# Optimization experiments

Hardware: AMD Instinct MI355X
Metric: run time of the kernel (lower is better)

The kernel has to match this reference:

```python
import math
import jax
import jax.numpy as jnp
import numpy as np

B = 2; Hrv = 16; Wrv = 1024; Crv = 64; Cb = 128; Cout = 128
D = 128; K = 5; NH = 8; NP = 4; DH = D // NH
Hbev = 220; Wbev = 220
RMAX = 55.0; XMIN = -55.0; XMAX = 55.0; YMIN = -55.0; YMAX = 55.0
EDGE_GAIN = 4.0; KLW = 1e-4

ELEV = np.array([-30.67, -29.33, -28.0, -26.66, -25.33, -24.0, -22.67, -21.33, -20.0, -18.67, -17.33, -16.0, -14.67, -13.33, -12.0, -10.67, -9.33, -8.0, -6.66, -5.33, -4.0, -2.67, -1.33, 0.0, 1.33, 2.67, 4.0, 5.33, 6.67, 8.0, 9.33, 10.67], dtype=np.float32)


def _buffers():
    groups = ELEV[::-1].reshape(Hrv, 32 // Hrv)
    steps = np.deg2rad(groups.max(1) - groups.min(1)).astype(np.float32)
    # torch Tensor.repeat == tile (faithful to original, even though rows end up interleaved)
    elev_steps = np.tile(steps, Wrv).reshape(Hrv, Wrv)
    means = np.deg2rad(groups.mean(1)).astype(np.float32)
    elevation = np.repeat(means, Wrv).reshape(Hrv, Wrv)  # numpy repeat == elementwise
    az_line = np.linspace(-np.pi, np.pi, Wrv + 1, dtype=np.float64)[:-1]
    az_step = float(az_line[1] - az_line[0])
    az_line = (az_line + az_step / 2).astype(np.float32)
    azimuth = np.broadcast_to(az_line[None, :], (Hrv, Wrv)).astype(np.float32).copy()
    offsets = np.linspace(-0.6, 0.6, K).astype(np.float32)
    u_vec = np.stack([np.cos(elevation) * np.cos(azimuth), np.cos(elevation) * np.sin(azimuth), np.sin(elevation)], 0).astype(np.float32)
    return (jnp.asarray(elev_steps), jnp.asarray(elevation), jnp.asarray(azimuth), az_step, jnp.asarray(offsets), jnp.asarray(u_vec))


def conv1x1(x, w, b):
    return jnp.einsum('bchw,oc->bohw', x, w) + b[None, :, None, None]


def groupnorm(x, g, gamma, beta, eps=1e-5):
    b_, c, h, w = x.shape
    xr = x.reshape(b_, g, c // g, h, w)
    m = xr.mean(axis=(2, 3, 4), keepdims=True)
    v = xr.var(axis=(2, 3, 4), keepdims=True)
    xn = ((xr - m) * jax.lax.rsqrt(v + eps)).reshape(b_, c, h, w)
    return xn * gamma[None, :, None, None] + beta[None, :, None, None]


def bilinear_sample(v_t, loc, H, W):
    # v_t: [B,NH,H*W,DH]; loc: [B,Nq,NH,NP,2] in [0,1]; grid_sample align_corners=False, zeros pad
    x = loc[..., 0] * W - 0.5
    y = loc[..., 1] * H - 0.5
    x0 = jnp.floor(x); y0 = jnp.floor(y)
    wx = x - x0; wy = y - y0
    x0i = x0.astype(jnp.int32); y0i = y0.astype(jnp.int32)
    b_, n_, nh_, p_ = x.shape

    def gather(xi, yi):
        valid = (xi >= 0) & (xi < W) & (yi >= 0) & (yi < H)
        idx = jnp.clip(yi, 0, H - 1) * W + jnp.clip(xi, 0, W - 1)
        idx_t = idx.transpose(0, 2, 1, 3).reshape(b_, nh_, n_ * p_)
        g = jnp.take_along_axis(v_t, idx_t[..., None], axis=2).reshape(b_, nh_, n_, p_, -1)
        return g * valid.transpose(0, 2, 1, 3)[..., None]

    wxt = wx.transpose(0, 2, 1, 3)[..., None]
    wyt = wy.transpose(0, 2, 1, 3)[..., None]
    g = gather(x0i, y0i) * (1 - wxt) * (1 - wyt)
    g = g + gather(x0i + 1, y0i) * wxt * (1 - wyt)
    g = g + gather(x0i, y0i + 1) * (1 - wxt) * wyt
    g = g + gather(x0i + 1, y0i + 1) * wxt * wyt
    return g  # [B,NH,Nq,NP,DH]


def setup_inputs():
    key = jax.random.key(0)
    ks = jax.random.split(key, 20)
    def rn(k, shape, s=0.02):
        return jax.random.normal(k, shape, jnp.float32) * s
    inp = {}
    inp['x_rv'] = jax.random.normal(ks[0], (B, Hrv, Wrv, Crv), jnp.float32)
    inp['bev'] = jax.random.normal(ks[1], (B, Cb, Hbev, Wbev), jnp.float32)
    inp['lidar2ego_mat'] = jnp.eye(4, dtype=jnp.float32)[None] + 0.01 * jax.random.normal(ks[2], (1, 4, 4), jnp.float32)
    inp['w_q'] = rn(ks[3], (D, Crv)); inp['b_q'] = jnp.zeros((D,), jnp.float32)
    inp['w_v'] = rn(ks[4], (D, Cb)); inp['b_v'] = jnp.zeros((D,), jnp.float32)
    inp['w_o'] = rn(ks[5], (Cout, D)); inp['b_o'] = jnp.zeros((Cout,), jnp.float32)
    inp['qs_w1'] = rn(ks[6], (D, D + 6)); inp['qs_b1'] = jnp.zeros((D,), jnp.float32)
    inp['qs_w2'] = rn(ks[7], (D, D)); inp['qs_b2'] = jnp.zeros((D,), jnp.float32)
    inp['rh_w1'] = rn(ks[8], (128, Crv + 3)); inp['rh_b1'] = jnp.zeros((128,), jnp.float32)
    inp['rh_g1'] = jnp.ones((128,), jnp.float32); inp['rh_bt1'] = jnp.zeros((128,), jnp.float32)
    inp['rh_w2'] = rn(ks[9], (64, 128, 3, 3))
    inp['rh_g2'] = jnp.ones((64,), jnp.float32); inp['rh_bt2'] = jnp.zeros((64,), jnp.float32)
    inp['rh_w3'] = rn(ks[10], (4, 64)); inp['rh_b3'] = jnp.zeros((4,), jnp.float32)
    inp['off_w'] = rn(ks[11], (NH * K * NP * 2, D)); inp['off_b'] = rn(ks[12], (NH * K * NP * 2,), 0.5)
    inp['aw_w'] = rn(ks[13], (NH * K * NP, D)); inp['aw_b'] = jnp.zeros((NH * K * NP,), jnp.float32)
    inp['val_w'] = rn(ks[14], (D, D)); inp['val_b'] = jnp.zeros((D,), jnp.float32)
    inp['out_w'] = rn(ks[15], (D, D)); inp['out_b'] = jnp.zeros((D,), jnp.float32)
    return inp


def reference(x_rv, bev, lidar2ego_mat, w_q, b_q, w_v, b_v, w_o, b_o, qs_w1, qs_b1, qs_w2, qs_b2, rh_w1, rh_b1, rh_g1, rh_bt1, rh_w2, rh_g2, rh_bt2, rh_w3, rh_b3, off_w, off_b, aw_w, aw_b, val_w, val_b, out_w, out_b):
    elev_steps, elevation, azimuth, az_step, offsets, u_vec = _buffers()
    x = jnp.transpose(x_rv, (0, 3, 1, 2))  # [B,Crv,Hrv,Wrv]
    Q0 = conv1x1(x, w_q, b_q)
    Vmap = conv1x1(bev, w_v, b_v)
    range_in = jnp.concatenate([x, jnp.broadcast_to(u_vec[None], (B, 3, Hrv, Wrv))], axis=1)
    h = jax.nn.gelu(groupnorm(conv1x1(range_in, rh_w1, rh_b1), 8, rh_g1, rh_bt1), approximate=False)
    hp = jnp.pad(h, ((0, 0), (0, 0), (1, 1), (1, 1)), mode='wrap')  # circular padding
    h = jax.lax.conv_general_dilated(hp, rh_w2, (1, 1), 'VALID', dimension_numbers=('NCHW', 'OIHW', 'NCHW'))
    h = jax.nn.gelu(groupnorm(h, 8, rh_g2, rh_bt2), approximate=False)
    head = conv1x1(h, rh_w3, rh_b3)  # [B,4,Hrv,Wrv]
    mu = jax.nn.sigmoid(head[:, 0:1]) * RMAX
    sd = jax.nn.softplus(head[:, 1:2]) + 1e-3
    se = jax.nn.sigmoid(head[:, 2:3]) * elev_steps + 1e-3
    sa = jax.nn.sigmoid(head[:, 3:4]) * az_step + 1e-3
    depth = mu[:, 0][..., None] + sd[:, 0][..., None] * offsets  # [B,Hrv,Wrv,K]
    elevs = elevation[None, :, :, None] + se[:, 0][..., None] * offsets
    azs = azimuth[None, :, :, None] + sa[:, 0][..., None] * offsets
    ce = jnp.cos(elevs)
    x_l = depth * ce * jnp.cos(azs)
    y_l = depth * ce * jnp.sin(azs)
    z_l = depth * jnp.sin(elevs)
    NK = Hrv * Wrv * K
    p = jnp.stack([x_l.reshape(B, NK), y_l.reshape(B, NK), z_l.reshape(B, NK), jnp.ones((B, NK), x_l.dtype)], axis=-1)
    p_ego = jnp.matmul(p, lidar2ego_mat)  # [B,NK,4]
    rx = jax.nn.sigmoid(EDGE_GAIN * ((p_ego[..., 0] - XMIN) / (XMAX - XMIN) - 0.5))
    ry = jax.nn.sigmoid(EDGE_GAIN * ((p_ego[..., 1] - YMIN) / (YMAX - YMIN) - 0.5))
    ref = jnp.stack([rx, ry], axis=-1).reshape(B, Hrv * Wrv, K, 2)
    sig_feat = jnp.concatenate([sd, se, sa, 1.0 / (sd + 1e-6), 1.0 / (se + 1e-6), 1.0 / (sa + 1e-6)], axis=1)
    Q = conv1x1(jax.nn.gelu(conv1x1(jnp.concatenate([Q0, sig_feat], axis=1), qs_w1, qs_b1), approximate=False), qs_w2, qs_b2)
    query = jnp.transpose(Q, (0, 2, 3, 1)).reshape(B, Hrv * Wrv, D)
    value = jnp.transpose(Vmap.reshape(B, D, Hbev * Wbev), (0, 2, 1))  # [B,HW,D]
    # MSDA -- all K levels share the same BEV value map (value was repeat(1,K,1))
    v = (value @ val_w.T + val_b).reshape(B, Hbev * Wbev, NH, DH)
    v_t = jnp.transpose(v, (0, 2, 1, 3))  # [B,NH,HW,DH]
    Nq = Hrv * Wrv
    smp_off = (query @ off_w.T + off_b).reshape(B, Nq, NH, K, NP, 2)
    attn = jax.nn.softmax((query @ aw_w.T + aw_b).reshape(B, Nq, NH, K * NP), axis=-1).reshape(B, Nq, NH, K, NP)
    norm = jnp.array([Wbev, Hbev], jnp.float32)
    loc = ref[:, :, None, :, None, :] + smp_off / norm  # [B,Nq,NH,K,NP,2]
    out = jnp.zeros((B, Nq, NH, DH), jnp.float32)
    for l in range(K):
        smp = bilinear_sample(v_t, loc[:, :, :, l], Hbev, Wbev)
        out = out + jnp.einsum('bhnpd,bnhp->bnhd', smp, attn[:, :, :, l])
    y_msda = out.reshape(B, Nq, D) @ out_w.T + out_b + query  # mmcv identity residual
    y = jnp.transpose(y_msda.reshape(B, Hrv, Wrv, D), (0, 3, 1, 2))
    y = conv1x1(y, w_o, b_o)
    mu_norm = mu / RMAX
    sr = jnp.maximum(sd, 1e-6)
    saz = sa / az_step
    sel = se / elev_steps
    L_kl = 0.5 * (mu_norm ** 2 + sr ** 2 - jnp.log(sr ** 2) - 1.0) \
         + 0.5 * (saz ** 2 - jnp.log(saz ** 2) - 1.0) \
         + 0.5 * (sel ** 2 - jnp.log(sel ** 2) - 1.0)
    kl = KLW * L_kl.mean()
    y = y.reshape(B, Hrv, Wrv, -1)  # faithful to torch .view on NCHW (no permute)
    return (y, kl)
```

## Files before the change

kernel.cpp:

```cpp
#include <hip/hip_runtime.h>
#include <math.h>

#define HRV 16
#define WRV 1024
#define NPIX 16384
#define NBEV 48400
#define BSZ 2

typedef __attribute__((ext_vector_type(8))) short short8;
typedef __attribute__((ext_vector_type(4))) float f32x4;

struct RVConsts {
  float steps[16];
  float means[16];
  float az_step_f;
  float pad_;
  double step_d;
  double az0;
  double az_half;
};

__device__ __forceinline__ float geluf(float x) {
  return 0.5f * x * (1.0f + erff(x * 0.70710678118654752440f));
}
__device__ __forceinline__ float sigmoidf_(float x) {
  return 1.0f / (1.0f + expf(-x));
}
__device__ __forceinline__ float softplusf_(float x) {
  return fmaxf(x, 0.0f) + log1pf(expf(-fabsf(x)));
}
__device__ __forceinline__ float azimf(int w, double step_d, double az0, double az_half) {
  double az = (double)w * step_d + az0;
  az += az_half;
  return (float)az;
}
__device__ __forceinline__ unsigned short f2bf(float f) {
  unsigned int u = __builtin_bit_cast(unsigned int, f);
  u = u + 0x7FFFu + ((u >> 16) & 1u);
  return (unsigned short)(u >> 16);
}
__device__ __forceinline__ float bf2f(unsigned short h) {
  unsigned int u = ((unsigned int)h) << 16;
  return __builtin_bit_cast(float, u);
}

__global__ __launch_bounds__(256) void k_rh1_q0(
    const float* __restrict__ x_rv,
    const unsigned short* __restrict__ rhW1p, const float* __restrict__ rh_b1,
    const unsigned short* __restrict__ wqp, const float* __restrict__ b_q,
    float* __restrict__ t1, unsigned short* __restrict__ q0,
    float* __restrict__ sums1, RVConsts C) {
  __shared__ unsigned short xin[64][104];
  __shared__ float wred[4][8][2];
  int b = blockIdx.y;
  int n0 = blockIdx.x * 64;
  int tid = threadIdx.x;
  const float* src = x_rv + ((size_t)b * NPIX + n0) * 64;
  for (int i = tid; i < 1024; i += 256) {
    int p = i >> 4, c = (i & 15) * 4;
    float4 v4 = *(const float4*)(src + p * 64 + c);
    xin[p][c] = f2bf(v4.x);
    xin[p][c + 1] = f2bf(v4.y);
    xin[p][c + 2] = f2bf(v4.z);
    xin[p][c + 3] = f2bf(v4.w);
  }
  if (tid < 64) {
    int n = n0 + tid;
    int h = n >> 10, w = n & 1023;
    float E = C.means[h];
    float A = azimf(w, C.step_d, C.az0, C.az_half);
    float ce = cosf(E);
    xin[tid][64] = f2bf(ce * cosf(A));
    xin[tid][65] = f2bf(ce * sinf(A));
    xin[tid][66] = f2bf(sinf(E));
    for (int c = 67; c < 104; c++) xin[tid][c] = 0;
  }
  __syncthreads();
  int wave = tid >> 6, l = tid & 63;
  int lr = l & 15, lk = l >> 4;
  f32x4 acc[8], accq[8];
#pragma unroll
  for (int nt = 0; nt < 8; nt++) {
    float b1 = rh_b1[nt * 16 + lr], b2 = b_q[nt * 16 + lr];
    acc[nt] = (f32x4){b1, b1, b1, b1};
    accq[nt] = (f32x4){b2, b2, b2, b2};
  }
#pragma unroll
  for (int ks = 0; ks < 3; ks++) {
    short8 a = *(const short8*)&xin[wave * 16 + lr][ks * 32 + lk * 8];
#pragma unroll
    for (int nt = 0; nt < 8; nt++) {
      short8 b1v = *(const short8*)(rhW1p + (size_t)(nt * 16 + lr) * 96 + ks * 32 + lk * 8);
      acc[nt] = __builtin_amdgcn_mfma_f32_16x16x32_bf16(a, b1v, acc[nt], 0, 0, 0);
      short8 b2v = *(const short8*)(wqp + (size_t)(nt * 16 + lr) * 96 + ks * 32 + lk * 8);
      accq[nt] = __builtin_amdgcn_mfma_f32_16x16x32_bf16(a, b2v, accq[nt], 0, 0, 0);
    }
  }
#pragma unroll
  for (int nt = 0; nt < 8; nt++) {
    int n = nt * 16 + lr;
#pragma unroll
    for (int r = 0; r < 4; r++) {
      int p = n0 + wave * 16 + lk * 4 + r;
      size_t o = ((size_t)b * NPIX + p) * 128 + n;
      t1[o] = acc[nt][r];
      q0[o] = f2bf(accq[nt][r]);
    }
  }
  float s1[8], ss1[8];
#pragma unroll
  for (int nt = 0; nt < 8; nt++) {
    float a0 = acc[nt][0], a1 = acc[nt][1], a2 = acc[nt][2], a3 = acc[nt][3];
    s1[nt] = a0 + a1 + a2 + a3;
    ss1[nt] = a0 * a0 + a1 * a1 + a2 * a2 + a3 * a3;
  }
#pragma unroll
  for (int nt = 0; nt < 8; nt++) {
    s1[nt] += __shfl_xor(s1[nt], 1);  ss1[nt] += __shfl_xor(ss1[nt], 1);
    s1[nt] += __shfl_xor(s1[nt], 2);  ss1[nt] += __shfl_xor(ss1[nt], 2);
    s1[nt] += __shfl_xor(s1[nt], 4);  ss1[nt] += __shfl_xor(ss1[nt], 4);
    s1[nt] += __shfl_xor(s1[nt], 8);  ss1[nt] += __shfl_xor(ss1[nt], 8);
    s1[nt] += __shfl_xor(s1[nt], 16); ss1[nt] += __shfl_xor(ss1[nt], 16);
    s1[nt] += __shfl_xor(s1[nt], 32); ss1[nt] += __shfl_xor(ss1[nt], 32);
  }
  if (l == 0) {
#pragma unroll
    for (int nt = 0; nt < 8; nt++) { wred[wave][nt][0] = s1[nt]; wred[wave][nt][1] = ss1[nt]; }
  }
  __syncthreads();
  if (tid < 8) {
    float S = wred[0][tid][0] + wred[1][tid][0] + wred[2][tid][0] + wred[3][tid][0];
    float SS = wred[0][tid][1] + wred[1][tid][1] + wred[2][tid][1] + wred[3][tid][1];
    sums1[(((size_t)b * 8 + tid) * 256 + blockIdx.x) * 2 + 0] = S;
    sums1[(((size_t)b * 8 + tid) * 256 + blockIdx.x) * 2 + 1] = SS;
  }
}

__device__ __forceinline__ int cswz2(int row, int colw, int c) {
  int byte = ((row * 10 + colw) << 8) + (c << 1);
  return byte ^ ((row & 7) << 4);
}
__global__ __launch_bounds__(256) void k_conv3g(
    const float* __restrict__ t1, const float* __restrict__ sums1,
    const float* __restrict__ g1, const float* __restrict__ bt1,
    const unsigned short* __restrict__ w2p,
    float* __restrict__ t2, float* __restrict__ sums2) {
  __shared__ unsigned short tile[16 * 10 * 128];
  __shared__ float st[8][2];
  __shared__ float wred[4][2][4][2];
  int b = blockIdx.y;
  int w0 = blockIdx.x * 8;
  int tid = threadIdx.x;
  if (tid < 8) {
    int g = tid;
    float S = 0.f, SS = 0.f;
    for (int ch = 0; ch < 256; ch++) {
      S += sums1[(((size_t)b * 8 + g) * 256 + ch) * 2];
      SS += sums1[(((size_t)b * 8 + g) * 256 + ch) * 2 + 1];
    }
    float m = S * (1.0f / 262144.0f);
    float var = SS * (1.0f / 262144.0f) - m * m;
    st[g][0] = m;
    st[g][1] = rsqrtf(var + 1e-5f);
  }
  __syncthreads();
  for (int i = tid; i < 5120; i += 256) {
    int row = i / 320;
    int rem = i - row * 320;
    int colw = rem >> 5;
    int c4 = (rem & 31) * 4;
    int wc = (w0 + colw - 1 + WRV) & (WRV - 1);
    float4 x4 = *(const float4*)(t1 + ((size_t)b * NPIX + row * WRV + wc) * 128 + c4);
    int g = c4 >> 4;
    float m = st[g][0], is = st[g][1];
    float4 g4 = *(const float4*)(g1 + c4);
    float4 b4 = *(const float4*)(bt1 + c4);
    float y0 = geluf((x4.x - m) * is * g4.x + b4.x);
    float y1 = geluf((x4.y - m) * is * g4.y + b4.y);
    float y2 = geluf((x4.z - m) * is * g4.z + b4.z);
    float y3 = geluf((x4.w - m) * is * g4.w + b4.w);
    uint2 o;
    o.x = (unsigned int)f2bf(y0) | ((unsigned int)f2bf(y1) << 16);
    o.y = (unsigned int)f2bf(y2) | ((unsigned int)f2bf(y3) << 16);
    *(uint2*)((char*)tile + cswz2(row, colw, c4)) = o;
  }
  __syncthreads();
  int wave = tid >> 6, l = tid & 63;
  int lr = l & 15, lk = l >> 4;
  f32x4 acc[2][4];
#pragma unroll
  for (int cc2 = 0; cc2 < 2; cc2++)
#pragma unroll
    for (int nt = 0; nt < 4; nt++) acc[cc2][nt] = (f32x4){0.f, 0.f, 0.f, 0.f};
#pragma unroll
  for (int kpos = 0; kpos < 9; kpos++) {
    int ky = kpos / 3, kx = kpos - ky * 3;
    int arow = (lr + ky - 1 + 16) & 15;
#pragma unroll
    for (int cc2 = 0; cc2 < 2; cc2++) {
      int acol = wave * 2 + cc2 + kx;
#pragma unroll
      for (int ks = 0; ks < 4; ks++) {
        short8 a = *(const short8*)((const char*)tile + cswz2(arow, acol, ks * 32 + lk * 8));
#pragma unroll
        for (int nt = 0; nt < 4; nt++) {
          short8 bv = *(const short8*)(w2p + (size_t)(kpos * 64 + nt * 16 + lr) * 128 +
                                       ks * 32 + lk * 8);
          acc[cc2][nt] = __builtin_amdgcn_mfma_f32_16x16x32_bf16(a, bv, acc[cc2][nt], 0, 0, 0);
        }
      }
    }
  }
#pragma unroll
  for (int cc2 = 0; cc2 < 2; cc2++) {
    int cc = wave * 2 + cc2;
#pragma unroll
    for (int nt = 0; nt < 4; nt++) {
      int o = nt * 16 + lr;
#pragma unroll
      for (int r = 0; r < 4; r++) {
        int p = (lk * 4 + r) * WRV + w0 + cc;
        t2[((size_t)b * NPIX + p) * 64 + o] = acc[cc2][nt][r];
      }
    }
  }
  float ps[4], pss[4];
#pragma unroll
  for (int nt = 0; nt < 4; nt++) { ps[nt] = 0.f; pss[nt] = 0.f; }
#pragma unroll
  for (int cc2 = 0; cc2 < 2; cc2++)
#pragma unroll
    for (int nt = 0; nt < 4; nt++)
#pragma unroll
      for (int r = 0; r < 4; r++) {
        float v = acc[cc2][nt][r];
        ps[nt] += v;
        pss[nt] += v * v;
      }
#pragma unroll
  for (int nt = 0; nt < 4; nt++) {
    ps[nt] += __shfl_xor(ps[nt], 1);  pss[nt] += __shfl_xor(pss[nt], 1);
    ps[nt] += __shfl_xor(ps[nt], 2);  pss[nt] += __shfl_xor(pss[nt], 2);
    ps[nt] += __shfl_xor(ps[nt], 4);  pss[nt] += __shfl_xor(pss[nt], 4);
    ps[nt] += __shfl_xor(ps[nt], 16); pss[nt] += __shfl_xor(pss[nt], 16);
    ps[nt] += __shfl_xor(ps[nt], 32); pss[nt] += __shfl_xor(pss[nt], 32);
  }
  if ((l & 0x37) == 0) {
    int b3 = (l >> 3) & 1;
#pragma unroll
    for (int nt = 0; nt < 4; nt++) {
      wred[wave][b3][nt][0] = ps[nt];
      wred[wave][b3][nt][1] = pss[nt];
    }
  }
  __syncthreads();
  if (tid < 8) {
    int nt = tid >> 1, b3 = tid & 1;
    float S = 0.f, SS = 0.f;
    for (int wv = 0; wv < 4; wv++) { S += wred[wv][b3][nt][0]; SS += wred[wv][b3][nt][1]; }
    int g = nt * 2 + b3;
    sums2[(((size_t)b * 8 + g) * 128 + blockIdx.x) * 2 + 0] = S;
    sums2[(((size_t)b * 8 + g) * 128 + blockIdx.x) * 2 + 1] = SS;
  }
}

__global__ __launch_bounds__(256) void k_headquery(
    const float* __restrict__ t2, const float* __restrict__ sums2,
    const float* __restrict__ g2, const float* __restrict__ bt2,
    const float* __restrict__ rh_w3, const float* __restrict__ rh_b3,
    const float* __restrict__ l2e, const unsigned short* __restrict__ q0,
    const unsigned short* __restrict__ qsW1p, const float* __restrict__ qs_b1,
    const float* __restrict__ qs_w1f,
    const unsigned short* __restrict__ qsW2p, const float* __restrict__ qs_b2,
    float* __restrict__ params, float* __restrict__ klpart,
    unsigned short* __restrict__ query, RVConsts C) {
  __shared__ float st2[8][2];
  __shared__ unsigned short qin[64][136];
  __shared__ unsigned short hq[64][136];
  __shared__ float sigf[64][6];
  __shared__ float klred[64];
  int b = blockIdx.y;
  int n0 = blockIdx.x * 64;
  int tid = threadIdx.x;
  if (tid < 8) {
    int g = tid;
    float S = 0.f, SS = 0.f;
    for (int ch = 0; ch < 128; ch++) {
      S += sums2[(((size_t)b * 8 + g) * 128 + ch) * 2];
      SS += sums2[(((size_t)b * 8 + g) * 128 + ch) * 2 + 1];
    }
    float m = S * (1.0f / 131072.0f);
    float var = SS * (1.0f / 131072.0f) - m * m;
    st2[g][0] = m;
    st2[g][1] = rsqrtf(var + 1e-5f);
  }
  const unsigned short* src = q0 + ((size_t)b * NPIX + n0) * 128;
  for (int i = tid; i < 1024; i += 256) {
    int p = i >> 4, c0 = (i & 15) * 8;
    *(uint4*)&qin[p][c0] = *(const uint4*)(src + p * 128 + c0);
  }
  __syncthreads();
  {
    int px = tid >> 2, q = tid & 3;
    int n = n0 + px;
    int h = n >> 10, w = n & 1023;
    const float* t = t2 + ((size_t)b * NPIX + n) * 64 + q * 16;
    float hd0 = 0.f, hd1 = 0.f, hd2 = 0.f, hd3 = 0.f;
#pragma unroll
    for (int j = 0; j < 16; j++) {
      int c = q * 16 + j;
      int g = c >> 3;
      float xv = geluf((t[j] - st2[g][0]) * st2[g][1] * g2[c] + bt2[c]);
      hd0 += rh_w3[c] * xv;
      hd1 += rh_w3[64 + c] * xv;
      hd2 += rh_w3[128 + c] * xv;
      hd3 += rh_w3[192 + c] * xv;
    }
    hd0 += __shfl_xor(hd0, 1); hd1 += __shfl_xor(hd1, 1);
    hd2 += __shfl_xor(hd2, 1); hd3 += __shfl_xor(hd3, 1);
    hd0 += __shfl_xor(hd0, 2); hd1 += __shfl_xor(hd1, 2);
    hd2 += __shfl_xor(hd2, 2); hd3 += __shfl_xor(hd3, 2);
    if (q == 0) {
      hd0 += rh_b3[0]; hd1 += rh_b3[1]; hd2 += rh_b3[2]; hd3 += rh_b3[3];
      float mu = sigmoidf_(hd0) * 55.0f;
      float sd = softplusf_(hd1) + 1e-3f;
      float stepw = C.steps[w & 15];
      float se = sigmoidf_(hd2) * stepw + 1e-3f;
      float sa = sigmoidf_(hd3) * C.az_step_f + 1e-3f;
      float E0 = C.means[h];
      float A0 = azimf(w, C.step_d, C.az0, C.az_half);
      float* P = params + ((size_t)b * NPIX + n) * 16;
      P[0] = sd; P[1] = se; P[2] = sa;
      sigf[px][0] = sd; sigf[px][1] = se; sigf[px][2] = sa;
      sigf[px][3] = 1.0f / (sd + 1e-6f);
      sigf[px][4] = 1.0f / (se + 1e-6f);
      sigf[px][5] = 1.0f / (sa + 1e-6f);
      float M00 = l2e[0], M01 = l2e[1], M10 = l2e[4], M11 = l2e[5];
      float M20 = l2e[8], M21 = l2e[9], M30 = l2e[12], M31 = l2e[13];
#pragma unroll
      for (int k = 0; k < 5; k++) {
        float off = -0.6f + 0.3f * (float)k;
        float d = mu + sd * off;
        float E = E0 + se * off;
        float A = A0 + sa * off;
        float ce = cosf(E);
        float xl = d * ce * cosf(A), yl = d * ce * sinf(A), zl = d * sinf(E);
        float px_ = xl * M00 + yl * M10 + zl * M20 + M30;
        float py_ = xl * M01 + yl * M11 + zl * M21 + M31;
        P[3 + 2 * k] = sigmoidf_(4.0f * ((px_ + 55.0f) * (1.0f / 110.0f) - 0.5f));
        P[4 + 2 * k] = sigmoidf_(4.0f * ((py_ + 55.0f) * (1.0f / 110.0f) - 0.5f));
      }
      float mu_n = mu * (1.0f / 55.0f);
      float sr = fmaxf(sd, 1e-6f);
      float saz = sa / C.az_step_f;
      float sel = se / stepw;
      klred[px] = 0.5f * (mu_n * mu_n + sr * sr - logf(sr * sr) - 1.0f) +
                  0.5f * (saz * saz - logf(saz * saz) - 1.0f) +
                  0.5f * (sel * sel - logf(sel * sel) - 1.0f);
    }
  }
  __syncthreads();
  if (tid == 0) {
    float sL = 0.f;
    for (int i = 0; i < 64; i++) sL += klred[i];
    klpart[b * 256 + blockIdx.x] = sL;
  }
  int wave = tid >> 6, l = tid & 63;
  int lr = l & 15, lk = l >> 4;
  f32x4 acc[8];
#pragma unroll
  for (int nt = 0; nt < 8; nt++) {
    int n = nt * 16 + lr;
    float wt[6];
#pragma unroll
    for (int c = 0; c < 6; c++) wt[c] = qs_w1f[(size_t)n * 134 + 128 + c];
    float bias = qs_b1[n];
#pragma unroll
    for (int r = 0; r < 4; r++) {
      int pl = wave * 16 + lk * 4 + r;
      float a = bias;
#pragma unroll
      for (int c = 0; c < 6; c++) a += wt[c] * sigf[pl][c];
      acc[nt][r] = a;
    }
  }
#pragma unroll
  for (int ks = 0; ks < 4; ks++) {
    short8 a = *(const short8*)&qin[wave * 16 + lr][ks * 32 + lk * 8];
#pragma unroll
    for (int nt = 0; nt < 8; nt++) {
      short8 bv = *(const short8*)(qsW1p + (size_t)(nt * 16 + lr) * 128 + ks * 32 + lk * 8);
      acc[nt] = __builtin_amdgcn_mfma_f32_16x16x32_bf16(a, bv, acc[nt], 0, 0, 0);
    }
  }
#pragma unroll
  for (int nt = 0; nt < 8; nt++)
#pragma unroll
    for (int r = 0; r < 4; r++)
      hq[wave * 16 + lk * 4 + r][nt * 16 + lr] = f2bf(geluf(acc[nt][r]));
  __syncthreads();
#pragma unroll
  for (int nt = 0; nt < 8; nt++) {
    float bias = qs_b2[nt * 16 + lr];
    acc[nt] = (f32x4){bias, bias, bias, bias};
  }
#pragma unroll
  for (int ks = 0; ks < 4; ks++) {
    short8 a = *(const short8*)&hq[wave * 16 + lr][ks * 32 + lk * 8];
#pragma unroll
    for (int nt = 0; nt < 8; nt++) {
      short8 bv = *(const short8*)(qsW2p + (size_t)(nt * 16 + lr) * 128 + ks * 32 + lk * 8);
      acc[nt] = __builtin_amdgcn_mfma_f32_16x16x32_bf16(a, bv, acc[nt], 0, 0, 0);
    }
  }
#pragma unroll
  for (int nt = 0; nt < 8; nt++) {
    int n = nt * 16 + lr;
#pragma unroll
    for (int r = 0; r < 4; r++) {
      int p = n0 + wave * 16 + lk * 4 + r;
      query[((size_t)b * NPIX + p) * 128 + n] = f2bf(acc[nt][r]);
    }
  }
}

__global__ __launch_bounds__(256) void k_pack(
    const float* __restrict__ val_w, const float* __restrict__ w_v,
    const float* __restrict__ b_v, const float* __restrict__ val_b,
    const float* __restrict__ off_w, const float* __restrict__ off_b,
    const float* __restrict__ aw_w, const float* __restrict__ aw_b,
    const float* __restrict__ out_w, const float* __restrict__ qs_w1,
    const float* __restrict__ qs_w2, const float* __restrict__ rh_w1,
    const float* __restrict__ w_q, const float* __restrict__ w_o,
    const float* __restrict__ rh_w2,
    unsigned short* __restrict__ wvv_bf, float* __restrict__ bvv,
    unsigned short* __restrict__ projW, float* __restrict__ projB,
    unsigned short* __restrict__ outW, unsigned short* __restrict__ qsW1p,
    unsigned short* __restrict__ qsW2p, unsigned short* __restrict__ rhW1p,
    unsigned short* __restrict__ wqp, unsigned short* __restrict__ woP,
    unsigned short* __restrict__ w2p) {
  int idx = blockIdx.x * 256 + threadIdx.x;
  if (idx < 16384) {
    int o = idx >> 7, c = idx & 127;
    float acc = 0.0f;
    for (int m = 0; m < 128; m++) acc += val_w[o * 128 + m] * w_v[m * 128 + c];
    wvv_bf[idx] = f2bf(acc);
  } else if (idx < 16512) {
    int o = idx - 16384;
    float acc = val_b[o];
    for (int m = 0; m < 128; m++) acc += val_w[o * 128 + m] * b_v[m];
    bvv[o] = acc;
  } else if (idx < 82048) {
    int j = idx - 16512;
    int r = j >> 7, c = j & 127;
    float w = (r < 320) ? off_w[r * 128 + c] : ((r < 480) ? aw_w[(r - 320) * 128 + c] : 0.0f);
    projW[j] = f2bf(w);
  } else if (idx < 82560) {
    int r = idx - 82048;
    projB[r] = (r < 320) ? off_b[r] : ((r < 480) ? aw_b[r - 320] : 0.0f);
  } else if (idx < 98944) {
    int j = idx - 82560;
    outW[j] = f2bf(out_w[j]);
  } else if (idx < 115328) {
    int j = idx - 98944;
    int r = j >> 7, c = j & 127;
    qsW1p[j] = f2bf(qs_w1[r * 134 + c]);
  } else if (idx < 131712) {
    int j = idx - 115328;
    qsW2p[j] = f2bf(qs_w2[j]);
  } else if (idx < 144000) {
    int j = idx - 131712;
    int r = j / 96, c = j - r * 96;
    rhW1p[j] = (c < 67) ? f2bf(rh_w1[r * 67 + c]) : 0;
  } else if (idx < 156288) {
    int j = idx - 144000;
    int r = j / 96, c = j - r * 96;
    wqp[j] = (c < 64) ? f2bf(w_q[r * 64 + c]) : 0;
  } else if (idx < 172672) {
    int j = idx - 156288;
    woP[j] = f2bf(w_o[j]);
  } else if (idx < 246400) {
    int j = idx - 172672;
    int kpos = j >> 13;
    int rem = j & 8191;
    int o = rem >> 7, c = rem & 127;
    int ky = kpos / 3, kx = kpos - ky * 3;
    w2p[j] = f2bf(rh_w2[((size_t)(o * 128 + c) * 3 + ky) * 3 + kx]);
  }
}

__global__ __launch_bounds__(256) void k_value(
    const float* __restrict__ bev, const unsigned short* __restrict__ wvv_bf,
    const float* __restrict__ bvv, unsigned short* __restrict__ v) {
  __shared__ float lds[128 * 66];
  int b = blockIdx.y;
  int p0 = blockIdx.x * 64;
  int tid = threadIdx.x;
  int npx = NBEV - p0; if (npx > 64) npx = 64;
  for (int i = tid; i < 128 * 64; i += 256) {
    int c = i >> 6, p = i & 63;
    lds[c * 66 + p] = (p < npx) ? bev[((size_t)b * 128 + c) * NBEV + p0 + p] : 0.0f;
  }
  __syncthreads();
  int wave = tid >> 6, l = tid & 63;
  int lr = l & 15, lk = l >> 4;
  int ploc = wave * 16 + lr;
  f32x4 acc[8];
#pragma unroll
  for (int nt = 0; nt < 8; nt++) {
    float bias = bvv[nt * 16 + lr];
    acc[nt] = (f32x4){bias, bias, bias, bias};
  }
#pragma unroll
  for (int ks = 0; ks < 4; ks++) {
    int k0 = ks * 32 + lk * 8;
    short8 a;
#pragma unroll
    for (int j = 0; j < 8; j++) a[j] = (short)f2bf(lds[(k0 + j) * 66 + ploc]);
#pragma unroll
    for (int nt = 0; nt < 8; nt++) {
      short8 bf = *(const short8*)(wvv_bf + (size_t)(nt * 16 + lr) * 128 + k0);
      acc[nt] = __builtin_amdgcn_mfma_f32_16x16x32_bf16(a, bf, acc[nt], 0, 0, 0);
    }
  }
#pragma unroll
  for (int nt = 0; nt < 8; nt++) {
    int n = nt * 16 + lr;
#pragma unroll
    for (int r = 0; r < 4; r++) {
      int p = p0 + wave * 16 + lk * 4 + r;
      if (p < NBEV) v[((size_t)b * NBEV + p) * 128 + n] = f2bf(acc[nt][r]);
    }
  }
}

__global__ __launch_bounds__(256) void k_proj(
    const unsigned short* __restrict__ query, const unsigned short* __restrict__ projW,
    const float* __restrict__ projB, unsigned short* __restrict__ proj) {
  __shared__ unsigned short qlds[64][136];
  int b = blockIdx.y;
  int p0b = blockIdx.x * 64;
  int tid = threadIdx.x;
  const unsigned short* src = query + ((size_t)b * NPIX + p0b) * 128;
  for (int i = tid; i < 1024; i += 256) {
    int p = i >> 4, c0 = (i & 15) * 8;
    *(uint4*)&qlds[p][c0] = *(const uint4*)(src + p * 128 + c0);
  }
  __syncthreads();
  int wave = tid >> 6, l = tid & 63;
  int lr = l & 15, lk = l >> 4;
  int p0 = p0b + wave * 16;
  for (int nc = 0; nc < 4; nc++) {
    int n0 = nc * 128;
    f32x4 acc[8];
#pragma unroll
    for (int nt = 0; nt < 8; nt++) {
      float bias = projB[n0 + nt * 16 + lr];
      acc[nt] = (f32x4){bias, bias, bias, bias};
    }
#pragma unroll
    for (int ks = 0; ks < 4; ks++) {
      short8 a = *(const short8*)&qlds[wave * 16 + lr][ks * 32 + lk * 8];
#pragma unroll
      for (int nt = 0; nt < 8; nt++) {
        short8 bf = *(const short8*)(projW + (size_t)(n0 + nt * 16 + lr) * 128 +
                                     ks * 32 + lk * 8);
        acc[nt] = __builtin_amdgcn_mfma_f32_16x16x32_bf16(a, bf, acc[nt], 0, 0, 0);
      }
    }
#pragma unroll
    for (int nt = 0; nt < 8; nt++) {
      int n = n0 + nt * 16 + lr;
#pragma unroll
      for (int r = 0; r < 4; r++) {
        int p = p0 + lk * 4 + r;
        proj[((size_t)b * NPIX + p) * 512 + n] = f2bf(acc[nt][r]);
      }
    }
  }
}

__global__ __launch_bounds__(256) void k_samp(
    const unsigned short* __restrict__ proj, const float* __restrict__ params,
    const unsigned short* __restrict__ v, unsigned short* __restrict__ S) {
  int b = blockIdx.y;
  int bid = blockIdx.x;
  int pb = (bid & 7) * 512 + (bid >> 3);
  int tid = threadIdx.x;
  int g = tid & 7;
  int hh = (tid >> 3) & 7;
  int pl = tid >> 6;
  int ts = g >> 1, th = g & 1;
  int n = pb * 4 + pl;
  const unsigned short* base = proj + ((size_t)b * NPIX + n) * 512;
  float lg[5];
#pragma unroll
  for (int t = 0; t < 5; t++) lg[t] = bf2f(base[320 + hh * 20 + ts * 5 + t]);
  float mx = fmaxf(fmaxf(fmaxf(lg[0], lg[1]), fmaxf(lg[2], lg[3])), lg[4]);
  mx = fmaxf(mx, __shfl_xor(mx, 2));
  mx = fmaxf(mx, __shfl_xor(mx, 4));
  float e[5];
  float s = 0.0f;
#pragma unroll
  for (int t = 0; t < 5; t++) { e[t] = expf(lg[t] - mx); s += e[t]; }
  s += __shfl_xor(s, 2);
  s += __shfl_xor(s, 4);
  float rs = 1.0f / s;
  const float* P = params + ((size_t)b * NPIX + n) * 16;
  const unsigned short* vb = v + (size_t)b * NBEV * 128 + hh * 16 + th * 8;
  float acc[8];
#pragma unroll
  for (int c = 0; c < 8; c++) acc[c] = 0.0f;
#pragma unroll
  for (int t = 0; t < 5; t++) {
    int kp = ts * 5 + t;
    int k = kp >> 2;
    unsigned int u = *(const unsigned int*)(base + hh * 40 + kp * 2);
    float X = P[3 + 2 * k] * 220.0f - 0.5f + bf2f((unsigned short)(u & 0xffffu));
    float Y = P[4 + 2 * k] * 220.0f - 0.5f + bf2f((unsigned short)(u >> 16));
    float xf = floorf(X), yf = floorf(Y);
    float wx = X - xf, wy = Y - yf;
    int x0 = (int)xf, y0 = (int)yf;
    float wx0 = ((unsigned)x0 < 220u) ? (1.0f - wx) : 0.0f;
    float wx1 = ((unsigned)(x0 + 1) < 220u) ? wx : 0.0f;
    float wy0 = ((unsigned)y0 < 220u) ? (1.0f - wy) : 0.0f;
    float wy1 = ((unsigned)(y0 + 1) < 220u) ? wy : 0.0f;
    int cx0 = min(max(x0, 0), 219), cx1 = min(max(x0 + 1, 0), 219);
    int cy0 = min(max(y0, 0), 219) * 220, cy1 = min(max(y0 + 1, 0), 219) * 220;
    float a = e[t] * rs;
    float u0 = a * wy0, u1 = a * wy1;
    float w4[4] = {u0 * wx0, u0 * wx1, u1 * wx0, u1 * wx1};
    int i4[4] = {cy0 + cx0, cy0 + cx1, cy1 + cx0, cy1 + cx1};
#pragma unroll
    for (int c2 = 0; c2 < 4; c2++) {
      float w = w4[c2];
      const uint2* sp = (const uint2*)(vb + (size_t)i4[c2] * 128);
      uint2 r0 = sp[0], r1 = sp[1];
      acc[0] += w * bf2f((unsigned short)(r0.x & 0xffffu));
      acc[1] += w * bf2f((unsigned short)(r0.x >> 16));
      acc[2] += w * bf2f((unsigned short)(r0.y & 0xffffu));
      acc[3] += w * bf2f((unsigned short)(r0.y >> 16));
      acc[4] += w * bf2f((unsigned short)(r1.x & 0xffffu));
      acc[5] += w * bf2f((unsigned short)(r1.x >> 16));
      acc[6] += w * bf2f((unsigned short)(r1.y & 0xffffu));
      acc[7] += w * bf2f((unsigned short)(r1.y >> 16));
    }
  }
#pragma unroll
  for (int c = 0; c < 8; c++) {
    acc[c] += __shfl_xor(acc[c], 2);
    acc[c] += __shfl_xor(acc[c], 4);
  }
  if (ts == 0) {
    uint4 o1;
    o1.x = (unsigned int)f2bf(acc[0]) | ((unsigned int)f2bf(acc[1]) << 16);
    o1.y = (unsigned int)f2bf(acc[2]) | ((unsigned int)f2bf(acc[3]) << 16);
    o1.z = (unsigned int)f2bf(acc[4]) | ((unsigned int)f2bf(acc[5]) << 16);
    o1.w = (unsigned int)f2bf(acc[6]) | ((unsigned int)f2bf(acc[7]) << 16);
    *(uint4*)(S + ((size_t)b * NPIX + n) * 128 + hh * 16 + th * 8) = o1;
  }
}

__global__ __launch_bounds__(256) void k_outfinal(
    const unsigned short* __restrict__ S, const unsigned short* __restrict__ outW,
    const float* __restrict__ out_b, const unsigned short* __restrict__ query,
    const unsigned short* __restrict__ woP, const float* __restrict__ b_o,
    const float* __restrict__ klpart, float* __restrict__ out) {
  __shared__ unsigned short ylds[64][136];
  __shared__ float yt[128][67];
  int b = blockIdx.y;
  int p0b = blockIdx.x * 64;
  int tid = threadIdx.x;
  int wave = tid >> 6, l = tid & 63;
  int lr = l & 15, lk = l >> 4;
  {
    f32x4 acc[8];
#pragma unroll
    for (int nt = 0; nt < 8; nt++) {
      float bias = out_b[nt * 16 + lr];
      acc[nt] = (f32x4){bias, bias, bias, bias};
    }
    const unsigned short* ap = S + ((size_t)b * NPIX + p0b + wave * 16 + lr) * 128 + lk * 8;
#pragma unroll
    for (int ks = 0; ks < 4; ks++) {
      short8 a = *(const short8*)(ap + ks * 32);
#pragma unroll
      for (int nt = 0; nt < 8; nt++) {
        short8 bf = *(const short8*)(outW + (size_t)(nt * 16 + lr) * 128 + ks * 32 + lk * 8);
        acc[nt] = __builtin_amdgcn_mfma_f32_16x16x32_bf16(a, bf, acc[nt], 0, 0, 0);
      }
    }
#pragma unroll
    for (int nt = 0; nt < 8; nt++) {
      int n = nt * 16 + lr;
#pragma unroll
      for (int r = 0; r < 4; r++) {
        int p_local = wave * 16 + lk * 4 + r;
        size_t o = ((size_t)b * NPIX + p0b + p_local) * 128 + n;
        ylds[p_local][n] = f2bf(acc[nt][r] + bf2f(query[o]));
      }
    }
  }
  __syncthreads();
  {
    f32x4 acc[8];
#pragma unroll
    for (int nt = 0; nt < 8; nt++) {
      float bias = b_o[nt * 16 + lr];
      acc[nt] = (f32x4){bias, bias, bias, bias};
    }
#pragma unroll
    for (int ks = 0; ks < 4; ks++) {
      short8 a = *(const short8*)&ylds[wave * 16 + lr][ks * 32 + lk * 8];
#pragma unroll
      for (int nt = 0; nt < 8; nt++) {
        short8 bf = *(const short8*)(woP + (size_t)(nt * 16 + lr) * 128 + ks * 32 + lk * 8);
        acc[nt] = __builtin_amdgcn_mfma_f32_16x16x32_bf16(a, bf, acc[nt], 0, 0, 0);
      }
    }
#pragma unroll
    for (int nt = 0; nt < 8; nt++)
#pragma unroll
      for (int r = 0; r < 4; r++)
        yt[nt * 16 + lr][wave * 16 + lk * 4 + r] = acc[nt][r];
  }
  __syncthreads();
  int n = tid >> 1, half = tid & 1;
  float* dst = out + ((size_t)(b * 128 + n)) * NPIX + p0b + half * 32;
#pragma unroll
  for (int j = 0; j < 8; j++) {
    float4 v4 = {yt[n][half * 32 + j * 4], yt[n][half * 32 + j * 4 + 1],
                 yt[n][half * 32 + j * 4 + 2], yt[n][half * 32 + j * 4 + 3]};
    *(float4*)(dst + j * 4) = v4;
  }
  if (blockIdx.x == 0 && b == 0 && tid == 0) {
    float sL = 0.0f;
    for (int i = 0; i < 512; i++) sL += klpart[i];
    out[(size_t)BSZ * 128 * NPIX] = 1e-4f * (sL / 32768.0f);
  }
}

static RVConsts make_consts() {
  static const float ELEV[32] = {
      -30.67f, -29.33f, -28.0f, -26.66f, -25.33f, -24.0f, -22.67f, -21.33f,
      -20.0f,  -18.67f, -17.33f, -16.0f, -14.67f, -13.33f, -12.0f, -10.67f,
      -9.33f,  -8.0f,   -6.66f,  -5.33f, -4.0f,   -2.67f,  -1.33f, 0.0f,
      1.33f,   2.67f,   4.0f,    5.33f,  6.67f,   8.0f,    9.33f,  10.67f};
  RVConsts C;
  const float d2r = 0.017453292519943295f;
  for (int r = 0; r < 16; r++) {
    float a = ELEV[31 - 2 * r], b = ELEV[30 - 2 * r];
    float mx = fmaxf(a, b), mn = fminf(a, b);
    C.steps[r] = (mx - mn) * d2r;
    C.means[r] = ((a + b) * 0.5f) * d2r;
  }
  const double PI_D = 3.14159265358979323846;
  double step_d = (PI_D - (-PI_D)) / 1024.0;
  double az0 = -PI_D;
  double az1 = az0 + step_d;
  double az_step_d = az1 - az0;
  C.az_step_f = (float)az_step_d;
  C.pad_ = 0.0f;
  C.step_d = step_d;
  C.az0 = az0;
  C.az_half = az_step_d * 0.5;
  return C;
}

#define OFF_T1     0u
#define OFF_T2     8388608u
#define OFF_Q0     10485760u
#define OFF_PARAMS 14680064u
#define OFF_QUERY  15204352u
#define OFF_S      19398656u
#define OFF_SUMS1  21495808u
#define OFF_SUMS2  21504000u
#define OFF_KL     21508096u
#define OFF_PROJ   0u
#define OFF_V      8388608u
#define OFF_WVV    21508608u
#define OFF_BVV    21516800u
#define OFF_PROJW  21516928u
#define OFF_PROJB  21549696u
#define OFF_OUTW   21550208u
#define OFF_QSW1   21558400u
#define OFF_QSW2   21566592u
#define OFF_RHW1   21574784u
#define OFF_WQP    21580928u
#define OFF_WOP    21587072u
#define OFF_W2P    21595264u

extern "C" void kernel_launch(void* const* d_in, const int* in_sizes, int n_in,
                              void* d_out, int out_size, void* d_ws, size_t ws_size,
                              hipStream_t stream) {
  const float* x_rv = (const float*)d_in[0];
  const float* bev = (const float*)d_in[1];
  const float* l2e = (const float*)d_in[2];
  const float* w_q = (const float*)d_in[3];
  const float* b_q = (const float*)d_in[4];
  const float* w_v = (const float*)d_in[5];
  const float* b_v = (const float*)d_in[6];
  const float* w_o = (const float*)d_in[7];
  const float* b_o = (const float*)d_in[8];
  const float* qs_w1 = (const float*)d_in[9];
  const float* qs_b1 = (const float*)d_in[10];
  const float* qs_w2 = (const float*)d_in[11];
  const float* qs_b2 = (const float*)d_in[12];
  const float* rh_w1 = (const float*)d_in[13];
  const float* rh_b1 = (const float*)d_in[14];
  const float* rh_g1 = (const float*)d_in[15];
  const float* rh_bt1 = (const float*)d_in[16];
  const float* rh_w2 = (const float*)d_in[17];
  const float* rh_g2 = (const float*)d_in[18];
  const float* rh_bt2 = (const float*)d_in[19];
  const float* rh_w3 = (const float*)d_in[20];
  const float* rh_b3 = (const float*)d_in[21];
  const float* off_w = (const float*)d_in[22];
  const float* off_b = (const float*)d_in[23];
  const float* aw_w = (const float*)d_in[24];
  const float* aw_b = (const float*)d_in[25];
  const float* val_w = (const float*)d_in[26];
  const float* val_b = (const float*)d_in[27];
  const float* out_w = (const float*)d_in[28];
  const float* out_b = (const float*)d_in[29];

  float* ws = (float*)d_ws;
  float* t1 = ws + OFF_T1;
  float* t2 = ws + OFF_T2;
  float* params = ws + OFF_PARAMS;
  float* sums1 = ws + OFF_SUMS1;
  float* sums2 = ws + OFF_SUMS2;
  float* klpart = ws + OFF_KL;
  float* bvv = ws + OFF_BVV;
  float* projB = ws + OFF_PROJB;
  unsigned short* q0bf = (unsigned short*)(ws + OFF_Q0);
  unsigned short* querybf = (unsigned short*)(ws + OFF_QUERY);
  unsigned short* S_bf = (unsigned short*)(ws + OFF_S);
  unsigned short* proj_bf = (unsigned short*)(ws + OFF_PROJ);
  unsigned short* v_bf = (unsigned short*)(ws + OFF_V);
  unsigned short* wvv_bf = (unsigned short*)(ws + OFF_WVV);
  unsigned short* projW = (unsigned short*)(ws + OFF_PROJW);
  unsigned short* outW = (unsigned short*)(ws + OFF_OUTW);
  unsigned short* qsW1p = (unsigned short*)(ws + OFF_QSW1);
  unsigned short* qsW2p = (unsigned short*)(ws + OFF_QSW2);
  unsigned short* rhW1p = (unsigned short*)(ws + OFF_RHW1);
  unsigned short* wqp = (unsigned short*)(ws + OFF_WQP);
  unsigned short* woP = (unsigned short*)(ws + OFF_WOP);
  unsigned short* w2p = (unsigned short*)(ws + OFF_W2P);

  RVConsts C = make_consts();
  dim3 blk(256);

  k_pack<<<963, blk, 0, stream>>>(val_w, w_v, b_v, val_b, off_w, off_b, aw_w, aw_b, out_w,
                                  qs_w1, qs_w2, rh_w1, w_q, w_o, rh_w2,
                                  wvv_bf, bvv, projW, projB, outW, qsW1p, qsW2p, rhW1p,
                                  wqp, woP, w2p);
  k_rh1_q0<<<dim3(256, BSZ), blk, 0, stream>>>(x_rv, rhW1p, rh_b1, wqp, b_q, t1, q0bf,
                                               sums1, C);
  k_conv3g<<<dim3(128, BSZ), blk, 0, stream>>>(t1, sums1, rh_g1, rh_bt1, w2p, t2, sums2);
  k_headquery<<<dim3(256, BSZ), blk, 0, stream>>>(t2, sums2, rh_g2, rh_bt2, rh_w3, rh_b3,
                                                  l2e, q0bf, qsW1p, qs_b1, qs_w1, qsW2p,
                                                  qs_b2, params, klpart, querybf, C);
  k_value<<<dim3(757, BSZ), blk, 0, stream>>>(bev, wvv_bf, bvv, v_bf);
  k_proj<<<dim3(256, BSZ), blk, 0, stream>>>(querybf, projW, projB, proj_bf);
  k_samp<<<dim3(4096, BSZ), blk, 0, stream>>>(proj_bf, params, v_bf, S_bf);
  k_outfinal<<<dim3(256, BSZ), blk, 0, stream>>>(S_bf, outW, out_b, querybf, woP, b_o,
                                                 klpart, (float*)d_out);
}
```

Measured before the change: 277.0 us.

## Enlarge k_value tile to 256 pixels with vectorized bf16 staging and swizzled LDS

The value-projection kernel now processes 256 BEV pixels per block instead of 64. It loads the input with float4 reads, converts to bf16 before storing into an XOR-swizzled LDS tile, and loops four 64-pixel sub-tiles through the MFMA path. This amortizes weight loads and block overhead, halves LDS footprint per pixel, and cuts scalar global loads. In exchange the grid shrinks to 380 blocks, which reduces parallelism on a large GPU, and LDS use grows to 64KB per block.

```diff
diff --git a/kernel.cpp b/kernel.cpp
--- a/kernel.cpp
+++ b/kernel.cpp
@@ -492,44 +492,68 @@
 __global__ __launch_bounds__(256) void k_value(
     const float* __restrict__ bev, const unsigned short* __restrict__ wvv_bf,
     const float* __restrict__ bvv, unsigned short* __restrict__ v) {
-  __shared__ float lds[128 * 66];
+  __shared__ unsigned short lds[128 * 256];
   int b = blockIdx.y;
-  int p0 = blockIdx.x * 64;
+  int p0 = blockIdx.x * 256;
   int tid = threadIdx.x;
-  int npx = NBEV - p0; if (npx > 64) npx = 64;
-  for (int i = tid; i < 128 * 64; i += 256) {
-    int c = i >> 6, p = i & 63;
-    lds[c * 66 + p] = (p < npx) ? bev[((size_t)b * 128 + c) * NBEV + p0 + p] : 0.0f;
+  for (int i = tid; i < 8192; i += 256) {
+    int c = i >> 6;
+    int p4 = (i & 63) * 4;
+    int p = p0 + p4;
+    float4 x;
+    if (p + 3 < NBEV) {
+      x = *(const float4*)(bev + ((size_t)b * 128 + c) * NBEV + p);
+    } else {
+      const float* row = bev + ((size_t)b * 128 + c) * NBEV;
+      x.x = (p + 0 < NBEV) ? row[p + 0] : 0.0f;
+      x.y = (p + 1 < NBEV) ? row[p + 1] : 0.0f;
+      x.z = (p + 2 < NBEV) ? row[p + 2] : 0.0f;
+      x.w = (p + 3 < NBEV) ? row[p + 3] : 0.0f;
+    }
+    uint2 o;
+    o.x = (unsigned int)f2bf(x.x) | ((unsigned int)f2bf(x.y) << 16);
+    o.y = (unsigned int)f2bf(x.z) | ((unsigned int)f2bf(x.w) << 16);
+    int byte = (c << 9) + (p4 << 1);
+    byte ^= ((c >> 3) & 7) << 4;
+    *(uint2*)((char*)lds + byte) = o;
   }
   __syncthreads();
   int wave = tid >> 6, l = tid & 63;
   int lr = l & 15, lk = l >> 4;
-  int ploc = wave * 16 + lr;
-  f32x4 acc[8];
-#pragma unroll
-  for (int nt = 0; nt < 8; nt++) {
-    float bias = bvv[nt * 16 + lr];
-    acc[nt] = (f32x4){bias, bias, bias, bias};
-  }
-#pragma unroll
-  for (int ks = 0; ks < 4; ks++) {
-    int k0 = ks * 32 + lk * 8;
-    short8 a;
-#pragma unroll
-    for (int j = 0; j < 8; j++) a[j] = (short)f2bf(lds[(k0 + j) * 66 + ploc]);
-#pragma unroll
-    for (int nt = 0; nt < 8; nt++) {
-      short8 bf = *(const short8*)(wvv_bf + (size_t)(nt * 16 + lr) * 128 + k0);
-      acc[nt] = __builtin_amdgcn_mfma_f32_16x16x32_bf16(a, bf, acc[nt], 0, 0, 0);
-    }
-  }
-#pragma unroll
-  for (int nt = 0; nt < 8; nt++) {
-    int n = nt * 16 + lr;
-#pragma unroll
-    for (int r = 0; r < 4; r++) {
-      int p = p0 + wave * 16 + lk * 4 + r;
-      if (p < NBEV) v[((size_t)b * NBEV + p) * 128 + n] = f2bf(acc[nt][r]);
+#pragma unroll
+  for (int sub = 0; sub < 4; sub++) {
+    int ploc = sub * 64 + wave * 16 + lr;
+    f32x4 acc[8];
+#pragma unroll
+    for (int nt = 0; nt < 8; nt++) {
+      float bias = bvv[nt * 16 + lr];
+      acc[nt] = (f32x4){bias, bias, bias, bias};
+    }
+#pragma unroll
+    for (int ks = 0; ks < 4; ks++) {
+      int k0 = ks * 32 + lk * 8;
+      short8 a;
+#pragma unroll
+      for (int j = 0; j < 8; j++) {
+        int k = k0 + j;
+        int byte = (k << 9) + (ploc << 1);
+        byte ^= ((k >> 3) & 7) << 4;
+        a[j] = *(const short*)((const char*)lds + byte);
+      }
+#pragma unroll
+      for (int nt = 0; nt < 8; nt++) {
+        short8 bf = *(const short8*)(wvv_bf + (size_t)(nt * 16 + lr) * 128 + k0);
+        acc[nt] = __builtin_amdgcn_mfma_f32_16x16x32_bf16(a, bf, acc[nt], 0, 0, 0);
+      }
+    }
+#pragma unroll
+    for (int nt = 0; nt < 8; nt++) {
+      int n = nt * 16 + lr;
+#pragma unroll
+      for (int r = 0; r < 4; r++) {
+        int p = p0 + sub * 64 + wave * 16 + lk * 4 + r;
+        if (p < NBEV) v[((size_t)b * NBEV + p) * 128 + n] = f2bf(acc[nt][r]);
+      }
     }
   }
 }
@@ -861,7 +885,7 @@
   k_headquery<<<dim3(256, BSZ), blk, 0, stream>>>(t2, sums2, rh_g2, rh_bt2, rh_w3, rh_b3,
                                                   l2e, q0bf, qsW1p, qs_b1, qs_w1, qsW2p,
                                                   qs_b2, params, klpart, querybf, C);
-  k_value<<<dim3(757, BSZ), blk, 0, stream>>>(bev, wvv_bf, bvv, v_bf);
+  k_value<<<dim3(190, BSZ), blk, 0, stream>>>(bev, wvv_bf, bvv, v_bf);
   k_proj<<<dim3(256, BSZ), blk, 0, stream>>>(querybf, projW, projB, proj_bf);
   k_samp<<<dim3(4096, BSZ), blk, 0, stream>>>(proj_bf, params, v_bf, S_bf);
   k_outfinal<<<dim3(256, BSZ), blk, 0, stream>>>(S_bf, outW, out_b, querybf, woP, b_o,
```

After: 270.8 us. -2.3%, faster.
